# Kernel optimization log

Measured on AMD Instinct MI355X. Metric: run time of the kernel, lower is better.

Reference implementation:

```python
import jax, jax.numpy as jnp
import numpy as np

GAMMA = 0.99      # discount_factor
LAM = 0.95        # gae_decay
CLIP = 0.2        # clipping_param
LOG_2PI = float(np.log(2.0 * np.pi))

B, T, A = 512, 2048, 16


def setup_inputs() -> dict:
    key = jax.random.key(0)
    ks = jax.random.split(key, 8)
    rewards = jax.random.normal(ks[0], (B, T), dtype=jnp.float32)
    critic_out = jax.random.normal(ks[1], (B, T + 1), dtype=jnp.float32)
    mu = jax.random.normal(ks[2], (B, T, A), dtype=jnp.float32)
    sigma = jax.random.uniform(ks[3], (B, T, A), dtype=jnp.float32) * 0.5 + 0.5
    old_mu = jax.random.normal(ks[4], (B, T, A), dtype=jnp.float32)
    old_sigma = jax.random.uniform(ks[5], (B, T, A), dtype=jnp.float32) * 0.5 + 0.5
    actions = jax.random.normal(ks[6], (B, T, A), dtype=jnp.float32)
    dones = jax.random.randint(ks[7], (B, T), 0, 2, dtype=jnp.int32)
    return {"rewards": rewards, "critic_out": critic_out, "mu": mu, "sigma": sigma,
            "old_mu": old_mu, "old_sigma": old_sigma, "actions": actions, "dones": dones}


def _normal_log_prob(x, mu, sigma):
    return -jnp.log(sigma) - 0.5 * LOG_2PI - 0.5 * jnp.square((x - mu) / sigma)


def _gae(rewards, dones_f, critic_out):
    # td_residuals: rewards + gamma * V[1:] - V[:-1]   -> [B, T]
    td = rewards + GAMMA * critic_out[:, 1:] - critic_out[:, :-1]
    b, t = rewards.shape
    # Reversed recurrence: adv[t] = td[t] + gamma*lam*(1 - done[t+1]) * adv[t+1],
    # for t = T-2 .. 0; adv[T-1] stays 0 (matches original loop bounds).
    xs = (jnp.flip(td[:, : t - 1], axis=1).T,        # [T-1, B]
          jnp.flip(dones_f[:, 1:], axis=1).T)        # [T-1, B]

    def step(carry, x):
        td_t, d_t = x
        adv = td_t + GAMMA * LAM * (1.0 - d_t) * carry
        return adv, adv

    _, advs = jax.lax.scan(step, jnp.zeros((b,), rewards.dtype), xs)
    advs = jnp.flip(advs, axis=0).T                  # [B, T-1]
    return jnp.concatenate([advs, jnp.zeros((b, 1), rewards.dtype)], axis=1)


def reference(rewards, critic_out, mu, sigma, old_mu, old_sigma, actions, dones):
    dones_f = dones.astype(rewards.dtype)
    advantages = _gae(rewards, dones_f, critic_out)          # [B, T]
    lp = _normal_log_prob(actions, mu, sigma)                # [B, T, A]
    old_lp = _normal_log_prob(actions, old_mu, old_sigma)    # [B, T, A]
    ratio = jnp.exp(lp - old_lp)
    clipped = jnp.minimum(jnp.maximum(ratio, 1.0 + CLIP), 1.0 - CLIP)
    adv = advantages[..., None]                              # broadcast over action dim
    obj = jnp.minimum(adv * ratio, adv * clipped)
    entropy = jnp.log(sigma) + 0.5 + 0.5 * LOG_2PI           # Normal entropy, [B, T, A]
    return jnp.mean(obj) + entropy
```

## Files before the change

### kernel.cpp

```cpp
#include <hip/hip_runtime.h>
#include <math.h>

#define BB 512
#define TT 2048
#define AA 16
#define NTOT (512LL * 2048LL * 16LL)
#define NV4  (NTOT / 4)
#define GAMMA 0.99f
#define GLAM  0.9405f
#define ENTC  1.4189385332046727f

#define NB2   4096
#define ITER2 4
#define S2    (NB2 * 256)

__global__ __launch_bounds__(256) void gae_kernel(
    const float* __restrict__ rewards, const float* __restrict__ vout,
    const int* __restrict__ dones, float* __restrict__ adv)
{
    const int b   = blockIdx.x;
    const int tid = threadIdx.x;
    const float* rw = rewards + (size_t)b * TT;
    const float* V  = vout    + (size_t)b * (TT + 1);
    const int*   dn = dones   + (size_t)b * TT;
    float*       av = adv     + (size_t)b * TT;

    const int tb = (TT - 8) - 8 * tid;

    const float4 r0 = ((const float4*)(rw + tb))[0];
    const float4 r1 = ((const float4*)(rw + tb))[1];
    const float4 v0 = ((const float4*)(V  + tb))[0];
    const float4 v1 = ((const float4*)(V  + tb))[1];
    const float  v8 = V[tb + 8];
    const int4   d0 = ((const int4*)(dn + tb))[0];
    const int4   d1 = ((const int4*)(dn + tb))[1];
    const int    d8 = (tid > 0) ? dn[tb + 8] : 0;

    float r_[8] = {r0.x, r0.y, r0.z, r0.w, r1.x, r1.y, r1.z, r1.w};
    float v_[9] = {v0.x, v0.y, v0.z, v0.w, v1.x, v1.y, v1.z, v1.w, v8};
    int   d_[9] = {d0.x, d0.y, d0.z, d0.w, d1.x, d1.y, d1.z, d1.w, d8};

    float ak[8], bk[8];
    float SA = 1.f, SB = 0.f;
    #pragma unroll
    for (int k = 0; k < 8; ++k) {
        const int j = 7 - k;
        float au, bu;
        if (tid == 0 && k == 0) { au = 0.f; bu = 0.f; }
        else {
            bu = r_[j] + GAMMA * v_[j + 1] - v_[j];
            au = GLAM * (1.f - (float)d_[j + 1]);
        }
        ak[k] = au; bk[k] = bu;
        SB = au * SB + bu;
        SA = au * SA;
    }

    const int lane = tid & 63;
    const int wave = tid >> 6;

    #pragma unroll
    for (int off = 1; off < 64; off <<= 1) {
        float pA = __shfl_up(SA, off, 64);
        float pB = __shfl_up(SB, off, 64);
        if (lane >= off) { SB = SA * pB + SB; SA = SA * pA; }
    }

    __shared__ float wA[4], wB[4];
    if (lane == 63) { wA[wave] = SA; wB[wave] = SB; }
    __syncthreads();

    float PA = 1.f, PB = 0.f;
    for (int w = 0; w < wave; ++w) {
        float aw = wA[w], bw = wB[w];
        PB = aw * PB + bw;
        PA = aw * PA;
    }

    float EA = __shfl_up(SA, 1, 64);
    float EB = __shfl_up(SB, 1, 64);
    if (lane == 0) { EA = 1.f; EB = 0.f; }

    float x = EA * PB + EB;
    float xv[8];
    #pragma unroll
    for (int k = 0; k < 8; ++k) {
        x = ak[k] * x + bk[k];
        xv[k] = x;
    }
    float4 o0 = {xv[7], xv[6], xv[5], xv[4]};
    float4 o1 = {xv[3], xv[2], xv[1], xv[0]};
    ((float4*)(av + tb))[0] = o0;
    ((float4*)(av + tb))[1] = o1;
}

__device__ __forceinline__ float obj1(float x, float m, float s,
                                      float om, float os, float ad)
{
    float rs  = __builtin_amdgcn_rcpf(s);
    float ros = __builtin_amdgcn_rcpf(os);
    float z   = (x - m) * rs;
    float zo  = (x - om) * ros;
    float d   = 0.5f * (zo * zo - z * z);
    float ratio = os * rs * __expf(d);
    return fminf(ad * ratio, ad * 0.8f);
}

__global__ __launch_bounds__(256) void obj_kernel(
    const float* __restrict__ mu, const float* __restrict__ sigma,
    const float* __restrict__ old_mu, const float* __restrict__ old_sigma,
    const float* __restrict__ actions, const float* __restrict__ adv,
    double* __restrict__ partials)
{
    const int tid = threadIdx.x;
    const size_t g = (size_t)blockIdx.x * 256 + tid;

    const float4* m4  = (const float4*)mu;
    const float4* s4  = (const float4*)sigma;
    const float4* om4 = (const float4*)old_mu;
    const float4* os4 = (const float4*)old_sigma;
    const float4* x4  = (const float4*)actions;

    float4 m[ITER2], s[ITER2], om[ITER2], os[ITER2], x[ITER2];
    float ad[ITER2];
    #pragma unroll
    for (int k = 0; k < ITER2; ++k) {
        size_t v = g + (size_t)k * S2;
        m[k]  = m4[v];
        s[k]  = s4[v];
        om[k] = om4[v];
        os[k] = os4[v];
        x[k]  = x4[v];
        ad[k] = adv[v >> 2];
    }

    float a0 = 0.f, a1 = 0.f, a2 = 0.f, a3 = 0.f;
    #pragma unroll
    for (int k = 0; k < ITER2; ++k) {
        a0 += obj1(x[k].x, m[k].x, s[k].x, om[k].x, os[k].x, ad[k]);
        a1 += obj1(x[k].y, m[k].y, s[k].y, om[k].y, os[k].y, ad[k]);
        a2 += obj1(x[k].z, m[k].z, s[k].z, om[k].z, os[k].z, ad[k]);
        a3 += obj1(x[k].w, m[k].w, s[k].w, om[k].w, os[k].w, ad[k]);
    }
    double lsum = ((double)a0 + (double)a1) + ((double)a2 + (double)a3);

    #pragma unroll
    for (int off = 32; off > 0; off >>= 1)
        lsum += __shfl_down(lsum, off, 64);

    __shared__ double wsum[4];
    const int lane = tid & 63, wave = tid >> 6;
    if (lane == 0) wsum[wave] = lsum;
    __syncthreads();
    if (tid == 0)
        partials[blockIdx.x] = wsum[0] + wsum[1] + wsum[2] + wsum[3];
}

__global__ __launch_bounds__(256) void reduce_kernel(
    const double* __restrict__ partials, float* __restrict__ meanOut)
{
    const int tid = threadIdx.x;
    double s = 0.0;
    for (int i = tid; i < NB2; i += 256) s += partials[i];
    #pragma unroll
    for (int off = 32; off > 0; off >>= 1)
        s += __shfl_down(s, off, 64);
    __shared__ double wsum[4];
    const int lane = tid & 63, wave = tid >> 6;
    if (lane == 0) wsum[wave] = s;
    __syncthreads();
    if (tid == 0) {
        double total = wsum[0] + wsum[1] + wsum[2] + wsum[3];
        meanOut[0] = (float)(total / (double)NTOT);
    }
}

__global__ __launch_bounds__(256) void out_kernel(
    const float* __restrict__ sigma, const float* __restrict__ meanPtr,
    float* __restrict__ out)
{
    const size_t g = (size_t)blockIdx.x * 256 + threadIdx.x;
    const float mean = meanPtr[0];
    const float4* s4 = (const float4*)sigma;
    float4* o4 = (float4*)out;
    #pragma unroll
    for (int k = 0; k < ITER2; ++k) {
        size_t v = g + (size_t)k * S2;
        float4 s = s4[v];
        float4 o;
        o.x = mean + __logf(s.x) + ENTC;
        o.y = mean + __logf(s.y) + ENTC;
        o.z = mean + __logf(s.z) + ENTC;
        o.w = mean + __logf(s.w) + ENTC;
        o4[v] = o;
    }
}

extern "C" void kernel_launch(void* const* d_in, const int* in_sizes, int n_in,
                              void* d_out, int out_size, void* d_ws, size_t ws_size,
                              hipStream_t stream) {
    const float* rewards   = (const float*)d_in[0];
    const float* critic    = (const float*)d_in[1];
    const float* mu        = (const float*)d_in[2];
    const float* sigma     = (const float*)d_in[3];
    const float* old_mu    = (const float*)d_in[4];
    const float* old_sigma = (const float*)d_in[5];
    const float* actions   = (const float*)d_in[6];
    const int*   dones     = (const int*)d_in[7];
    float* out = (float*)d_out;

    char* ws = (char*)d_ws;
    float*  meanPtr  = (float*)ws;
    double* partials = (double*)(ws + 256);
    float*  adv      = (float*)(ws + 65536);

    gae_kernel<<<BB, 256, 0, stream>>>(rewards, critic, dones, adv);
    obj_kernel<<<NB2, 256, 0, stream>>>(mu, sigma, old_mu, old_sigma,
                                        actions, adv, partials);
    reduce_kernel<<<1, 256, 0, stream>>>(partials, meanPtr);
    out_kernel<<<NB2, 256, 0, stream>>>(sigma, meanPtr, out);
}
```

Measured before the change: 346.3 us.

## Use one float4 per thread and reverse out_kernel block order for cache reuse

The objective and output kernels now process one float4 per thread across 16384 blocks instead of four strided float4s over 4096 blocks. This removes per-thread unrolled loads and raises the block count. The output kernel also walks blocks in reverse, so the tail of sigma, read last by the objective kernel, is read again while it may still sit in cache. The cost is fewer loads in flight per thread, more partial sums to reduce, and a larger workspace for partials.

```diff
diff --git a/kernel.cpp b/kernel.cpp
--- a/kernel.cpp
+++ b/kernel.cpp
@@ -3,16 +3,12 @@
 
 #define BB 512
 #define TT 2048
-#define AA 16
 #define NTOT (512LL * 2048LL * 16LL)
 #define NV4  (NTOT / 4)
+#define NB2  16384
 #define GAMMA 0.99f
 #define GLAM  0.9405f
 #define ENTC  1.4189385332046727f
-
-#define NB2   4096
-#define ITER2 4
-#define S2    (NB2 * 256)
 
 __global__ __launch_bounds__(256) void gae_kernel(
     const float* __restrict__ rewards, const float* __restrict__ vout,
@@ -36,9 +32,9 @@
     const int4   d1 = ((const int4*)(dn + tb))[1];
     const int    d8 = (tid > 0) ? dn[tb + 8] : 0;
 
-    float r_[8] = {r0.x, r0.y, r0.z, r0.w, r1.x, r1.y, r1.z, r1.w};
-    float v_[9] = {v0.x, v0.y, v0.z, v0.w, v1.x, v1.y, v1.z, v1.w, v8};
-    int   d_[9] = {d0.x, d0.y, d0.z, d0.w, d1.x, d1.y, d1.z, d1.w, d8};
+    float r_[8] = {r0.x,r0.y,r0.z,r0.w,r1.x,r1.y,r1.z,r1.w};
+    float v_[9] = {v0.x,v0.y,v0.z,v0.w,v1.x,v1.y,v1.z,v1.w,v8};
+    int   d_[9] = {d0.x,d0.y,d0.z,d0.w,d1.x,d1.y,d1.z,d1.w,d8};
 
     float ak[8], bk[8];
     float SA = 1.f, SB = 0.f;
@@ -113,36 +109,20 @@
     double* __restrict__ partials)
 {
     const int tid = threadIdx.x;
-    const size_t g = (size_t)blockIdx.x * 256 + tid;
+    const size_t v = (size_t)blockIdx.x * 256 + tid;
 
-    const float4* m4  = (const float4*)mu;
-    const float4* s4  = (const float4*)sigma;
-    const float4* om4 = (const float4*)old_mu;
-    const float4* os4 = (const float4*)old_sigma;
-    const float4* x4  = (const float4*)actions;
+    float4 m  = ((const float4*)mu)[v];
+    float4 s  = ((const float4*)sigma)[v];
+    float4 om = ((const float4*)old_mu)[v];
+    float4 os = ((const float4*)old_sigma)[v];
+    float4 x  = ((const float4*)actions)[v];
+    float  ad = adv[v >> 2];
 
-    float4 m[ITER2], s[ITER2], om[ITER2], os[ITER2], x[ITER2];
-    float ad[ITER2];
-    #pragma unroll
-    for (int k = 0; k < ITER2; ++k) {
-        size_t v = g + (size_t)k * S2;
-        m[k]  = m4[v];
-        s[k]  = s4[v];
-        om[k] = om4[v];
-        os[k] = os4[v];
-        x[k]  = x4[v];
-        ad[k] = adv[v >> 2];
-    }
-
-    float a0 = 0.f, a1 = 0.f, a2 = 0.f, a3 = 0.f;
-    #pragma unroll
-    for (int k = 0; k < ITER2; ++k) {
-        a0 += obj1(x[k].x, m[k].x, s[k].x, om[k].x, os[k].x, ad[k]);
-        a1 += obj1(x[k].y, m[k].y, s[k].y, om[k].y, os[k].y, ad[k]);
-        a2 += obj1(x[k].z, m[k].z, s[k].z, om[k].z, os[k].z, ad[k]);
-        a3 += obj1(x[k].w, m[k].w, s[k].w, om[k].w, os[k].w, ad[k]);
-    }
-    double lsum = ((double)a0 + (double)a1) + ((double)a2 + (double)a3);
+    float o = obj1(x.x, m.x, s.x, om.x, os.x, ad)
+            + obj1(x.y, m.y, s.y, om.y, os.y, ad)
+            + obj1(x.z, m.z, s.z, om.z, os.z, ad)
+            + obj1(x.w, m.w, s.w, om.w, os.w, ad);
+    double lsum = (double)o;
 
     #pragma unroll
     for (int off = 32; off > 0; off >>= 1)
@@ -179,21 +159,15 @@
     const float* __restrict__ sigma, const float* __restrict__ meanPtr,
     float* __restrict__ out)
 {
-    const size_t g = (size_t)blockIdx.x * 256 + threadIdx.x;
+    const size_t v = (size_t)(NB2 - 1 - blockIdx.x) * 256 + threadIdx.x;
     const float mean = meanPtr[0];
-    const float4* s4 = (const float4*)sigma;
-    float4* o4 = (float4*)out;
-    #pragma unroll
-    for (int k = 0; k < ITER2; ++k) {
-        size_t v = g + (size_t)k * S2;
-        float4 s = s4[v];
-        float4 o;
-        o.x = mean + __logf(s.x) + ENTC;
-        o.y = mean + __logf(s.y) + ENTC;
-        o.z = mean + __logf(s.z) + ENTC;
-        o.w = mean + __logf(s.w) + ENTC;
-        o4[v] = o;
-    }
+    float4 s = ((const float4*)sigma)[v];
+    float4 o;
+    o.x = mean + (__logf(s.x) + ENTC);
+    o.y = mean + (__logf(s.y) + ENTC);
+    o.z = mean + (__logf(s.z) + ENTC);
+    o.w = mean + (__logf(s.w) + ENTC);
+    ((float4*)out)[v] = o;
 }
 
 extern "C" void kernel_launch(void* const* d_in, const int* in_sizes, int n_in,
@@ -211,8 +185,8 @@
 
     char* ws = (char*)d_ws;
     float*  meanPtr  = (float*)ws;
-    double* partials = (double*)(ws + 256);
-    float*  adv      = (float*)(ws + 65536);
+    double* partials = (double*)(ws + 1024);
+    float*  adv      = (float*)(ws + 1024 + 131072);
 
     gae_kernel<<<BB, 256, 0, stream>>>(rewards, critic, dones, adv);
     obj_kernel<<<NB2, 256, 0, stream>>>(mu, sigma, old_mu, old_sigma,
```

Result: no change. 353.0 us (+1.9%).
